# Kernel optimization log

Hardware: AMD Instinct MI355X
Metric: run time of the kernel (lower is better)

The kernel has to match this reference:

```python
import jax, jax.numpy as jnp
import numpy as np

D_MODEL = 256
NHEAD = 8
HEAD_DIM = D_MODEL // NHEAD
EPS = 1e-6
LN_EPS = 1e-5


def embed_rotary(x, cos, sin):
    # x, cos, sin: [N, L, C]; rotate even/odd pairs (Lepard-style RoFPE)
    x2 = jnp.stack([-x[..., 1::2], x[..., ::2]], axis=-1).reshape(x.shape)
    return x * cos + x2 * sin


def layer_norm(x, g, b):
    m = jnp.mean(x, axis=-1, keepdims=True)
    v = jnp.mean((x - m) ** 2, axis=-1, keepdims=True)
    return (x - m) / jnp.sqrt(v + LN_EPS) * g + b


def setup_inputs() -> dict:
    key = jax.random.key(0)
    ks = jax.random.split(key, 12)
    N, L, S, C = 8, 4096, 4096, D_MODEL
    s = 1.0 / np.sqrt(C)
    return {
        "x": jax.random.normal(ks[0], (N, L, C), jnp.float32),
        "source": jax.random.normal(ks[1], (N, S, C), jnp.float32),
        "x_pe": jax.random.normal(ks[2], (N, L, C, 2), jnp.float32),
        "source_pe": jax.random.normal(ks[3], (N, S, C, 2), jnp.float32),
        "Wq": jax.random.normal(ks[4], (C, C), jnp.float32) * s,
        "Wk": jax.random.normal(ks[5], (C, C), jnp.float32) * s,
        "Wv": jax.random.normal(ks[6], (C, C), jnp.float32) * s,
        "Wm": jax.random.normal(ks[7], (C, C), jnp.float32) * s,
        "W1": jax.random.normal(ks[8], (2 * C, 2 * C), jnp.float32) * s,
        "W2": jax.random.normal(ks[9], (2 * C, C), jnp.float32) * s,
        "ln1_g": jnp.ones((C,), jnp.float32),
        "ln1_b": jnp.zeros((C,), jnp.float32),
        "ln2_g": jnp.ones((C,), jnp.float32),
        "ln2_b": jnp.zeros((C,), jnp.float32),
    }


def reference(x, source, x_pe, source_pe, Wq, Wk, Wv, Wm, W1, W2, ln1_g, ln1_b, ln2_g, ln2_b):
    N, L, C = x.shape
    S = source.shape[1]
    H, D = NHEAD, HEAD_DIM

    query = x @ Wq           # [N, L, C]
    key = source @ Wk        # [N, S, C]
    value = source @ Wv      # [N, S, C]

    # ELU+1 feature maps (on pre-rotary projections)
    Q = jax.nn.elu(query) + 1.0
    K = jax.nn.elu(key) + 1.0

    q_cos, q_sin = x_pe[..., 0], x_pe[..., 1]
    k_cos, k_sin = source_pe[..., 0], source_pe[..., 1]
    Q_pos = embed_rotary(query, q_cos, q_sin)
    K_pos = embed_rotary(key, k_cos, k_sin)
    value = embed_rotary(value, k_cos, k_sin)

    Q = Q.reshape(N, L, H, D)
    K = K.reshape(N, S, H, D)
    Q_pos = Q_pos.reshape(N, L, H, D)
    K_pos = K_pos.reshape(N, S, H, D)
    value = value.reshape(N, S, H, D)

    values = value / S
    KV = jnp.einsum('nshd,nshv->nhdv', K_pos, values)          # [N, H, D, D]
    Z = 1.0 / (jnp.einsum('nlhd,nhd->nlh', Q, K.sum(axis=1)) + EPS)
    queried = jnp.einsum('nlhd,nhdv->nlhv', Q_pos, KV) * Z[..., None] * S  # [N, L, H, D]

    message = queried.reshape(N, L, C) @ Wm
    message = layer_norm(message, ln1_g, ln1_b)
    h = jnp.concatenate([x, message], axis=2) @ W1             # [N, L, 2C]
    h = jax.nn.relu(h)
    message = h @ W2                                            # [N, L, C]
    message = layer_norm(message, ln2_g, ln2_b)
    return x + message
```

## Files before the change

kernel.cpp:

```cpp
#include <hip/hip_runtime.h>

typedef __attribute__((ext_vector_type(8))) short bf16x8;
typedef __attribute__((ext_vector_type(4))) float f32x4;

__device__ __forceinline__ float bf2f(unsigned short b) {
    unsigned u = ((unsigned)b) << 16; float f;
    __builtin_memcpy(&f, &u, 4); return f;
}
__device__ __forceinline__ unsigned short f2bf(float f) {
    unsigned u; __builtin_memcpy(&u, &f, 4);
    unsigned r = u + 0x7FFFu + ((u >> 16) & 1u);
    return (unsigned short)(r >> 16);
}
__device__ __forceinline__ unsigned packbf(float a, float b) {
    return (unsigned)f2bf(a) | ((unsigned)f2bf(b) << 16);
}
__device__ __forceinline__ float elu1(float v) { return v > 0.f ? v + 1.f : __expf(v); }

__device__ __forceinline__ void async_copy16(const unsigned short* g, unsigned short* l) {
    __builtin_amdgcn_global_load_lds(
        (const __attribute__((address_space(1))) unsigned int*)g,
        (__attribute__((address_space(3))) unsigned int*)l, 16, 0, 0);
}

__device__ __host__ __forceinline__ int chan_of(int tc) {
    return (tc & ~63) | ((tc & 15) << 1) | ((tc >> 4) & 1) | (((tc >> 5) & 1) << 5);
}
__device__ __forceinline__ int chan_even(int gnb, int p, int low) {
    const int tc = gnb + 32 * p + low;
    return (tc & ~63) | ((tc & 15) << 1) | (((tc >> 5) & 1) << 5);
}

#define EPI_RELU 0
#define EPI_Q 1
#define EPI_KV 2
#define EPI_LN1 3
#define EPI_LN2RES 4

template <int MT, int NT, int EPI>
__global__ __launch_bounds__(256) void gemm_bt(
    const unsigned short* __restrict__ A, int lda,
    const unsigned short* __restrict__ B, int K,
    unsigned short* __restrict__ Cb, int ldc,
    const float* __restrict__ pe,
    const float* __restrict__ KsumC, float* __restrict__ KsumA,
    float* __restrict__ Zbuf, unsigned short* __restrict__ Qpos,
    unsigned short* __restrict__ KF, unsigned short* __restrict__ VF,
    const float* __restrict__ g, const float* __restrict__ bta,
    unsigned short* __restrict__ A2out,
    const float* __restrict__ xres, float* __restrict__ outF)
{
    constexpr int WM = MT / 2, WN = NT / 2, MI = WM / 16, NI = WN / 16;
    constexpr int LPS = 1 + NT / 64;
    constexpr int PF = (NT == 128) ? 4 : 2;
    constexpr int RD = PF + 1;
    static_assert(MT == 64, "A staging assumes MT*4 == 256 chunks");
    __shared__ unsigned short Asm[RD][MT * 32];
    __shared__ unsigned short Bsm[RD][NT * 32];
    const int t = threadIdx.x;
    const int lane = t & 63, w = t >> 6;
    const int wm = w & 1, wn = w >> 1;
    const int quad = lane >> 4, low = lane & 15;
    const int m0 = blockIdx.x * MT, n0 = blockIdx.y * NT;

    f32x4 acc[MI][NI];
#pragma unroll
    for (int i = 0; i < MI; i++)
#pragma unroll
        for (int j = 0; j < NI; j++) acc[i][j] = (f32x4){0.f, 0.f, 0.f, 0.f};

    auto stage = [&](int k0, int buf) {
        {
            const int row = t >> 2;
            const int part = (t & 3) ^ ((t >> 3) & 3);
            async_copy16(A + (size_t)(m0 + row) * lda + k0 + part * 8,
                         &Asm[buf][(w * 64) * 8]);
        }
#pragma unroll
        for (int i = 0; i < NT / 64; i++) {
            const int chunk = i * 256 + t;
            const int row = chunk >> 2;
            const int part = (chunk & 3) ^ ((chunk >> 3) & 3);
            async_copy16(B + (size_t)(n0 + row) * K + k0 + part * 8,
                         &Bsm[buf][(i * 256 + w * 64) * 8]);
        }
    };

    const int nk = K >> 5;
    const int swz = (low >> 1) & 3;
#pragma unroll
    for (int i = 0; i < PF; i++) stage(i << 5, i);
    int kb = 0, sb = PF;
    for (int ks = 0; ks < nk; ks++) {
        const int rem = nk - 1 - ks;
        __builtin_amdgcn_sched_barrier(0);
        if constexpr (PF == 4) {
            if (rem >= 3)      asm volatile("s_waitcnt vmcnt(9)" ::: "memory");
            else if (rem == 2) asm volatile("s_waitcnt vmcnt(6)" ::: "memory");
            else if (rem == 1) asm volatile("s_waitcnt vmcnt(3)" ::: "memory");
            else               asm volatile("s_waitcnt vmcnt(0)" ::: "memory");
        } else {
            if (rem >= 1)      asm volatile("s_waitcnt vmcnt(5)" ::: "memory");
            else               asm volatile("s_waitcnt vmcnt(0)" ::: "memory");
        }
        __builtin_amdgcn_s_barrier();
        __builtin_amdgcn_sched_barrier(0);
        if (ks + PF < nk) stage((ks + PF) << 5, sb);
        bf16x8 a[MI], b[NI];
#pragma unroll
        for (int mi = 0; mi < MI; mi++)
            a[mi] = *(const bf16x8*)&Asm[kb][(wm * WM + mi * 16 + low) * 32 + ((quad ^ swz)) * 8];
#pragma unroll
        for (int ni = 0; ni < NI; ni++)
            b[ni] = *(const bf16x8*)&Bsm[kb][(wn * WN + ni * 16 + low) * 32 + ((quad ^ swz)) * 8];
#pragma unroll
        for (int mi = 0; mi < MI; mi++)
#pragma unroll
            for (int ni = 0; ni < NI; ni++)
                acc[mi][ni] = __builtin_amdgcn_mfma_f32_16x16x32_bf16(a[mi], b[ni], acc[mi][ni], 0, 0, 0);
        kb = (kb + 1 == RD) ? 0 : kb + 1;
        sb = (sb + 1 == RD) ? 0 : sb + 1;
    }

    const int gmb = m0 + wm * WM, gnb = n0 + wn * WN;

    if constexpr (EPI == EPI_RELU) {
#pragma unroll
        for (int mi = 0; mi < MI; mi++)
#pragma unroll
            for (int p = 0; p < NI / 2; p++) {
                const int c_e = chan_even(gnb, p, low);
#pragma unroll
                for (int r = 0; r < 4; r++) {
                    const int row = gmb + mi * 16 + quad * 4 + r;
                    const float ve = acc[mi][2 * p][r], vo = acc[mi][2 * p + 1][r];
                    *(unsigned*)&Cb[(size_t)row * ldc + c_e] =
                        packbf(ve > 0.f ? ve : 0.f, vo > 0.f ? vo : 0.f);
                }
            }
    } else if constexpr (EPI == EPI_Q) {
        const int n = m0 >> 12;
#pragma unroll
        for (int p = 0; p < NI / 2; p++) {
            const int c_e = chan_even(gnb, p, low);
            const int head = c_e >> 5;
            const float2 ks = *(const float2*)&KsumC[n * 256 + c_e];
#pragma unroll
            for (int mi = 0; mi < MI; mi++) {
#pragma unroll
                for (int r = 0; r < 4; r++) {
                    const int row = gmb + mi * 16 + quad * 4 + r;
                    const float4 cs = *(const float4*)&pe[((size_t)row * 256 + c_e) * 2];
                    const float ve = acc[mi][2 * p][r], vo = acc[mi][2 * p + 1][r];
                    *(unsigned*)&Qpos[(size_t)row * 256 + c_e] =
                        packbf(ve * cs.x - vo * cs.y, vo * cs.z + ve * cs.w);
                    float z = elu1(ve) * ks.x + elu1(vo) * ks.y;
                    z += __shfl_xor(z, 1); z += __shfl_xor(z, 2);
                    z += __shfl_xor(z, 4); z += __shfl_xor(z, 8);
                    if (low == 0) Zbuf[(size_t)row * 8 + head] = 1.f / (z + 1e-6f);
                }
            }
        }
    } else if constexpr (EPI == EPI_KV) {
        const int n = m0 >> 12;
#pragma unroll
        for (int p = 0; p < NI / 2; p++) {
            const int tcg = gnb + 32 * p;
            const bool isK = ((tcg >> 5) & 1) == 0;
            const int c = ((tcg & ~63) >> 1) | (low << 1);
            const int nh = n * 8 + (c >> 5), d = c & 31;
            unsigned short* dst = isK ? KF : VF;
            float kel_e = 0.f, kel_o = 0.f;
#pragma unroll
            for (int mi = 0; mi < MI; mi++) {
                const int row0 = gmb + mi * 16 + quad * 4;
                const int s0 = row0 & 4095;
                unsigned short pk[8];
#pragma unroll
                for (int r = 0; r < 4; r++) {
                    const int row = row0 + r;
                    const float4 cs = *(const float4*)&pe[((size_t)row * 256 + c) * 2];
                    const float ve = acc[mi][2 * p][r], vo = acc[mi][2 * p + 1][r];
                    pk[r]     = f2bf(ve * cs.x - vo * cs.y);
                    pk[4 + r] = f2bf(vo * cs.z + ve * cs.w);
                    if (isK) { kel_e += elu1(ve); kel_o += elu1(vo); }
                }
                const size_t base = ((size_t)nh * 512 + (s0 >> 3)) * 32;
                *(uint2*)&dst[(base + d) * 8 + (s0 & 7)]     = *(const uint2*)&pk[0];
                *(uint2*)&dst[(base + d + 1) * 8 + (s0 & 7)] = *(const uint2*)&pk[4];
            }
            if (isK) {
                kel_e += __shfl_xor(kel_e, 16); kel_e += __shfl_xor(kel_e, 32);
                kel_o += __shfl_xor(kel_o, 16); kel_o += __shfl_xor(kel_o, 32);
                if (quad == 0) {
                    atomicAdd(&KsumA[n * 256 + c], kel_e);
                    atomicAdd(&KsumA[n * 256 + c + 1], kel_o);
                }
            }
        }
    } else {
        __shared__ float2 lnp[2][64];
#pragma unroll
        for (int mi = 0; mi < MI; mi++)
#pragma unroll
            for (int r = 0; r < 4; r++) {
                float s1 = 0.f, s2 = 0.f;
#pragma unroll
                for (int ni = 0; ni < NI; ni++) {
                    const float v = acc[mi][ni][r];
                    s1 += v; s2 += v * v;
                }
                s1 += __shfl_xor(s1, 1); s2 += __shfl_xor(s2, 1);
                s1 += __shfl_xor(s1, 2); s2 += __shfl_xor(s2, 2);
                s1 += __shfl_xor(s1, 4); s2 += __shfl_xor(s2, 4);
                s1 += __shfl_xor(s1, 8); s2 += __shfl_xor(s2, 8);
                if (low == 0) lnp[wn][wm * WM + mi * 16 + quad * 4 + r] = make_float2(s1, s2);
            }
        __syncthreads();
#pragma unroll
        for (int mi = 0; mi < MI; mi++)
#pragma unroll
            for (int r = 0; r < 4; r++) {
                const int rl = wm * WM + mi * 16 + quad * 4 + r;
                const int row = m0 + rl;
                const float2 pa = lnp[0][rl], pb = lnp[1][rl];
                const float mean = (pa.x + pb.x) * (1.f / 256.f);
                const float var = (pa.y + pb.y) * (1.f / 256.f) - mean * mean;
                const float rstd = rsqrtf(var + 1e-5f);
#pragma unroll
                for (int p = 0; p < NI / 2; p++) {
                    const int c_e = chan_even(gnb, p, low);
                    const float2 gg = *(const float2*)&g[c_e];
                    const float2 bb = *(const float2*)&bta[c_e];
                    const float ve = acc[mi][2 * p][r], vo = acc[mi][2 * p + 1][r];
                    const float oe = (ve - mean) * rstd * gg.x + bb.x;
                    const float oo = (vo - mean) * rstd * gg.y + bb.y;
                    if constexpr (EPI == EPI_LN1) {
                        *(unsigned*)&A2out[(size_t)row * 512 + 256 + c_e] = packbf(oe, oo);
                    } else {
                        const float2 xv = *(const float2*)&xres[(size_t)row * 256 + c_e];
                        float2 o; o.x = xv.x + oe; o.y = xv.y + oo;
                        *(float2*)&outF[(size_t)row * 256 + c_e] = o;
                    }
                }
            }
    }
}

__global__ void prep_weights(const float* __restrict__ Wq, const float* __restrict__ Wk,
                             const float* __restrict__ Wv, const float* __restrict__ Wm,
                             const float* __restrict__ W1, const float* __restrict__ W2,
                             unsigned short* __restrict__ WqT, unsigned short* __restrict__ WkvT,
                             unsigned short* __restrict__ WmT, unsigned short* __restrict__ W1T,
                             unsigned short* __restrict__ W2T, float* __restrict__ zero_base) {
    const int idx = blockIdx.x * 256 + threadIdx.x;
    if (idx < 65536) {
        const int tc = idx >> 8, k = idx & 255;
        WqT[idx] = f2bf(Wq[(size_t)k * 256 + chan_of(tc)]);
    } else if (idx < 196608) {
        const int i = idx - 65536, tc = i >> 8, k = i & 255;
        const int f = (tc >> 5) & 1;
        const int c = ((tc & ~63) >> 1) | ((tc & 15) << 1) | ((tc >> 4) & 1);
        WkvT[i] = f2bf(f ? Wv[(size_t)k * 256 + c] : Wk[(size_t)k * 256 + c]);
    } else if (idx < 262144) {
        const int i = idx - 196608, tc = i >> 8, k = i & 255;
        WmT[i] = f2bf(Wm[(size_t)k * 256 + chan_of(tc)]);
    } else if (idx < 524288) {
        const int i = idx - 262144, tc = i >> 9, k = i & 511;
        W1T[i] = f2bf(W1[(size_t)k * 512 + chan_of(tc)]);
    } else if (idx < 655360) {
        const int i = idx - 524288, tc = i >> 9, k = i & 511;
        W2T[i] = f2bf(W2[(size_t)k * 256 + chan_of(tc)]);
    } else {
        zero_base[idx - 655360] = 0.f;
    }
}

__global__ void conv_bf16(const float* __restrict__ src, unsigned short* __restrict__ dst, int dstride) {
    const int idx = blockIdx.x * 256 + threadIdx.x;
    const int row = idx >> 6;
    const int c0 = (idx & 63) * 4;
    const float4 v = *(const float4*)&src[(size_t)row * 256 + c0];
    unsigned short o[4] = {f2bf(v.x), f2bf(v.y), f2bf(v.z), f2bf(v.w)};
    *(uint2*)&dst[(size_t)row * dstride + c0] = *(const uint2*)o;
}

__global__ __launch_bounds__(256) void kv2_kernel(const unsigned short* __restrict__ KF,
                                                  const unsigned short* __restrict__ VF,
                                                  float* __restrict__ KVT) {
    const int nh = blockIdx.x, sc = blockIdx.y;
    const int t = threadIdx.x, lane = t & 63, w = t >> 6;
    const int quad = lane >> 4, low = lane & 15;
    const int sbase = sc * 1024 + w * 256;

    f32x4 acc[2][2];
#pragma unroll
    for (int i = 0; i < 2; i++)
#pragma unroll
        for (int j = 0; j < 2; j++) acc[i][j] = (f32x4){0.f, 0.f, 0.f, 0.f};

    for (int s0 = 0; s0 < 256; s0 += 32) {
        const int sk = sbase + s0 + quad * 8;
        const size_t cb = ((size_t)nh * 512 + (sk >> 3)) * 32;
        bf16x8 a[2], b[2];
#pragma unroll
        for (int mi = 0; mi < 2; mi++)
            a[mi] = *(const bf16x8*)&KF[(cb + mi * 16 + low) * 8];
#pragma unroll
        for (int ni = 0; ni < 2; ni++)
            b[ni] = *(const bf16x8*)&VF[(cb + ni * 16 + low) * 8];
#pragma unroll
        for (int mi = 0; mi < 2; mi++)
#pragma unroll
            for (int ni = 0; ni < 2; ni++)
                acc[mi][ni] = __builtin_amdgcn_mfma_f32_16x16x32_bf16(a[mi], b[ni], acc[mi][ni], 0, 0, 0);
    }

    __shared__ float red[4][1024];
#pragma unroll
    for (int mi = 0; mi < 2; mi++)
#pragma unroll
        for (int ni = 0; ni < 2; ni++)
#pragma unroll
            for (int r = 0; r < 4; r++)
                red[w][(mi * 16 + quad * 4 + r) * 32 + ni * 16 + low] = acc[mi][ni][r];
    __syncthreads();
#pragma unroll
    for (int k = 0; k < 4; k++) {
        const int i = t + k * 256;
        const float s = red[0][i] + red[1][i] + red[2][i] + red[3][i];
        atomicAdd(&KVT[(size_t)nh * 1024 + (size_t)(i & 31) * 32 + (i >> 5)], s);
    }
}

__global__ __launch_bounds__(256) void attn_out_kernel(const unsigned short* __restrict__ Qpos,
                                                       const float* __restrict__ KVT,
                                                       const float* __restrict__ Zbuf,
                                                       unsigned short* __restrict__ Qrd) {
    const int h = blockIdx.y, mt = blockIdx.x;
    const int t = threadIdx.x, lane = t & 63, w = t >> 6;
    const int quad = lane >> 4, low = lane & 15;
    const int rbase = mt * 256 + w * 64;
    const int n = rbase >> 12;

    bf16x8 b[2];
#pragma unroll
    for (int ni = 0; ni < 2; ni++) {
        const float* src = &KVT[((size_t)(n * 8 + h) * 32 + ni * 16 + low) * 32 + quad * 8];
        short tmp[8];
#pragma unroll
        for (int j = 0; j < 8; j++) tmp[j] = (short)f2bf(src[j]);
        __builtin_memcpy(&b[ni], tmp, 16);
    }

    f32x4 acc[4][2];
#pragma unroll
    for (int i = 0; i < 4; i++)
#pragma unroll
        for (int j = 0; j < 2; j++) acc[i][j] = (f32x4){0.f, 0.f, 0.f, 0.f};

#pragma unroll
    for (int mi = 0; mi < 4; mi++) {
        const bf16x8 a = *(const bf16x8*)&Qpos[((size_t)(rbase + mi * 16 + low)) * 256 + h * 32 + quad * 8];
#pragma unroll
        for (int ni = 0; ni < 2; ni++)
            acc[mi][ni] = __builtin_amdgcn_mfma_f32_16x16x32_bf16(a, b[ni], acc[mi][ni], 0, 0, 0);
    }

#pragma unroll
    for (int mi = 0; mi < 4; mi++)
#pragma unroll
        for (int ni = 0; ni < 2; ni++)
#pragma unroll
            for (int r = 0; r < 4; r++) {
                const int row = rbase + mi * 16 + quad * 4 + r;
                const int col = h * 32 + ni * 16 + low;
                Qrd[(size_t)row * 256 + col] = f2bf(acc[mi][ni][r] * Zbuf[(size_t)row * 8 + h]);
            }
}

extern "C" void kernel_launch(void* const* d_in, const int* in_sizes, int n_in,
                              void* d_out, int out_size, void* d_ws, size_t ws_size,
                              hipStream_t stream) {
    const float* x   = (const float*)d_in[0];
    const float* src = (const float*)d_in[1];
    const float* xpe = (const float*)d_in[2];
    const float* spe = (const float*)d_in[3];
    const float* Wq  = (const float*)d_in[4];
    const float* Wk  = (const float*)d_in[5];
    const float* Wv  = (const float*)d_in[6];
    const float* Wm  = (const float*)d_in[7];
    const float* W1  = (const float*)d_in[8];
    const float* W2  = (const float*)d_in[9];
    const float* g1  = (const float*)d_in[10];
    const float* b1  = (const float*)d_in[11];
    const float* g2  = (const float*)d_in[12];
    const float* b2  = (const float*)d_in[13];

    char* p = (char*)d_ws;
    unsigned short* WqT  = (unsigned short*)p; p += 256 * 256 * 2;
    unsigned short* WkvT = (unsigned short*)p; p += 512 * 256 * 2;
    unsigned short* WmT  = (unsigned short*)p; p += 256 * 256 * 2;
    unsigned short* W1T  = (unsigned short*)p; p += 512 * 512 * 2;
    unsigned short* W2T  = (unsigned short*)p; p += 256 * 512 * 2;
    float* KVT  = (float*)p; p += 64 * 1024 * 4;
    float* Ksum = (float*)p; p += 8 * 256 * 4;
    float* Zbuf = (float*)p; p += (size_t)32768 * 8 * 4;
    unsigned short* A2   = (unsigned short*)p; p += (size_t)32768 * 512 * 2;
    unsigned short* srcB = (unsigned short*)p; p += (size_t)32768 * 256 * 2;
    unsigned short* KF   = (unsigned short*)p; p += (size_t)32768 * 256 * 2;
    unsigned short* VF   = (unsigned short*)p; p += (size_t)32768 * 256 * 2;
    unsigned short* Qpos = (unsigned short*)p; p += (size_t)32768 * 256 * 2;
    unsigned short* Qrd  = (unsigned short*)p; p += (size_t)32768 * 256 * 2;
    unsigned short* hbuf = KF;

    prep_weights<<<2824, 256, 0, stream>>>(Wq, Wk, Wv, Wm, W1, W2,
                                           WqT, WkvT, WmT, W1T, W2T, KVT);
    conv_bf16<<<8192, 256, 0, stream>>>(x, A2, 512);
    conv_bf16<<<8192, 256, 0, stream>>>(src, srcB, 256);

    gemm_bt<64, 128, EPI_KV><<<dim3(512, 4), 256, 0, stream>>>(
        srcB, 256, WkvT, 256, nullptr, 0, spe, nullptr, Ksum,
        nullptr, nullptr, KF, VF, nullptr, nullptr, nullptr, nullptr, nullptr);
    kv2_kernel<<<dim3(64, 4), 256, 0, stream>>>(KF, VF, KVT);

    gemm_bt<64, 128, EPI_Q><<<dim3(512, 2), 256, 0, stream>>>(
        A2, 512, WqT, 256, nullptr, 0, xpe, Ksum, nullptr,
        Zbuf, Qpos, nullptr, nullptr, nullptr, nullptr, nullptr, nullptr, nullptr);

    attn_out_kernel<<<dim3(128, 8), 256, 0, stream>>>(Qpos, KVT, Zbuf, Qrd);

    gemm_bt<64, 256, EPI_LN1><<<512, 256, 0, stream>>>(
        Qrd, 256, WmT, 256, nullptr, 0, nullptr, nullptr, nullptr,
        nullptr, nullptr, nullptr, nullptr, g1, b1, A2, nullptr, nullptr);

    gemm_bt<64, 128, EPI_RELU><<<dim3(512, 4), 256, 0, stream>>>(
        A2, 512, W1T, 512, hbuf, 512, nullptr, nullptr, nullptr,
        nullptr, nullptr, nullptr, nullptr, nullptr, nullptr, nullptr, nullptr, nullptr);

    gemm_bt<64, 256, EPI_LN2RES><<<512, 256, 0, stream>>>(
        hbuf, 512, W2T, 512, nullptr, 0, nullptr, nullptr, nullptr,
        nullptr, nullptr, nullptr, nullptr, g2, b2, nullptr, x, (float*)d_out);
}
```

Before: 414.6 us.

## Fuse FFN W1+ReLU and W2+LayerNorm+residual into one kernel with LDS hidden tile

Replaces the two separate FFN GEMM launches with a single 512-thread kernel. Each block computes a 64x512 ReLU hidden tile into swizzled LDS, then multiplies it by W2 and applies LayerNorm and the residual add. This removes the 32 MB bf16 hidden-activation round trip through global memory and one launch. In exchange it uses large LDS (about 136 KB per block), which limits occupancy, and it uses shallow double buffering with full vmcnt(0) waits. It also changes the prefetch depth for NT=128 GEMMs from 4 to 2 and adjusts the wait counts to match.

```diff
diff --git a/kernel.cpp b/kernel.cpp
--- a/kernel.cpp
+++ b/kernel.cpp
@@ -31,28 +31,24 @@
     return (tc & ~63) | ((tc & 15) << 1) | (((tc >> 5) & 1) << 5);
 }
 
-#define EPI_RELU 0
 #define EPI_Q 1
 #define EPI_KV 2
 #define EPI_LN1 3
-#define EPI_LN2RES 4
 
 template <int MT, int NT, int EPI>
 __global__ __launch_bounds__(256) void gemm_bt(
     const unsigned short* __restrict__ A, int lda,
     const unsigned short* __restrict__ B, int K,
-    unsigned short* __restrict__ Cb, int ldc,
     const float* __restrict__ pe,
     const float* __restrict__ KsumC, float* __restrict__ KsumA,
     float* __restrict__ Zbuf, unsigned short* __restrict__ Qpos,
     unsigned short* __restrict__ KF, unsigned short* __restrict__ VF,
     const float* __restrict__ g, const float* __restrict__ bta,
-    unsigned short* __restrict__ A2out,
-    const float* __restrict__ xres, float* __restrict__ outF)
+    unsigned short* __restrict__ A2out)
 {
     constexpr int WM = MT / 2, WN = NT / 2, MI = WM / 16, NI = WN / 16;
     constexpr int LPS = 1 + NT / 64;
-    constexpr int PF = (NT == 128) ? 4 : 2;
+    constexpr int PF = 2;
     constexpr int RD = PF + 1;
     static_assert(MT == 64, "A staging assumes MT*4 == 256 chunks");
     __shared__ unsigned short Asm[RD][MT * 32];
@@ -94,10 +90,8 @@
     for (int ks = 0; ks < nk; ks++) {
         const int rem = nk - 1 - ks;
         __builtin_amdgcn_sched_barrier(0);
-        if constexpr (PF == 4) {
-            if (rem >= 3)      asm volatile("s_waitcnt vmcnt(9)" ::: "memory");
-            else if (rem == 2) asm volatile("s_waitcnt vmcnt(6)" ::: "memory");
-            else if (rem == 1) asm volatile("s_waitcnt vmcnt(3)" ::: "memory");
+        if constexpr (LPS == 3) {
+            if (rem >= 1)      asm volatile("s_waitcnt vmcnt(3)" ::: "memory");
             else               asm volatile("s_waitcnt vmcnt(0)" ::: "memory");
         } else {
             if (rem >= 1)      asm volatile("s_waitcnt vmcnt(5)" ::: "memory");
@@ -124,21 +118,7 @@
 
     const int gmb = m0 + wm * WM, gnb = n0 + wn * WN;
 
-    if constexpr (EPI == EPI_RELU) {
-#pragma unroll
-        for (int mi = 0; mi < MI; mi++)
-#pragma unroll
-            for (int p = 0; p < NI / 2; p++) {
-                const int c_e = chan_even(gnb, p, low);
-#pragma unroll
-                for (int r = 0; r < 4; r++) {
-                    const int row = gmb + mi * 16 + quad * 4 + r;
-                    const float ve = acc[mi][2 * p][r], vo = acc[mi][2 * p + 1][r];
-                    *(unsigned*)&Cb[(size_t)row * ldc + c_e] =
-                        packbf(ve > 0.f ? ve : 0.f, vo > 0.f ? vo : 0.f);
-                }
-            }
-    } else if constexpr (EPI == EPI_Q) {
+    if constexpr (EPI == EPI_Q) {
         const int n = m0 >> 12;
 #pragma unroll
         for (int p = 0; p < NI / 2; p++) {
@@ -235,16 +215,174 @@
                     const float ve = acc[mi][2 * p][r], vo = acc[mi][2 * p + 1][r];
                     const float oe = (ve - mean) * rstd * gg.x + bb.x;
                     const float oo = (vo - mean) * rstd * gg.y + bb.y;
-                    if constexpr (EPI == EPI_LN1) {
-                        *(unsigned*)&A2out[(size_t)row * 512 + 256 + c_e] = packbf(oe, oo);
-                    } else {
-                        const float2 xv = *(const float2*)&xres[(size_t)row * 256 + c_e];
-                        float2 o; o.x = xv.x + oe; o.y = xv.y + oo;
-                        *(float2*)&outF[(size_t)row * 256 + c_e] = o;
-                    }
+                    *(unsigned*)&A2out[(size_t)row * 512 + 256 + c_e] = packbf(oe, oo);
                 }
             }
     }
+}
+
+__global__ __launch_bounds__(512) void ffn_kernel(
+    const unsigned short* __restrict__ A2,
+    const unsigned short* __restrict__ W1T,
+    const unsigned short* __restrict__ W2T,
+    const float* __restrict__ g, const float* __restrict__ bta,
+    const float* __restrict__ xres, float* __restrict__ outF)
+{
+    __shared__ unsigned short Hs[64 * 512];
+    __shared__ unsigned short Bst[2][512 * 32];
+    __shared__ unsigned short Ast[2][64 * 32];
+    __shared__ float2 lnp[4][64];
+    const int t = threadIdx.x;
+    const int lane = t & 63, w = t >> 6;
+    const int wm = w & 1, wn = w >> 1;
+    const int quad = lane >> 4, low = lane & 15;
+    const int m0 = blockIdx.x * 64;
+    const int swz = (low >> 1) & 3;
+
+    f32x4 acc[2][8];
+#pragma unroll
+    for (int i = 0; i < 2; i++)
+#pragma unroll
+        for (int j = 0; j < 8; j++) acc[i][j] = (f32x4){0.f, 0.f, 0.f, 0.f};
+
+    auto stage1 = [&](int k0, int buf) {
+        if (w < 4) {
+            const int row = t >> 2;
+            const int part = (t & 3) ^ ((t >> 3) & 3);
+            async_copy16(A2 + (size_t)(m0 + row) * 512 + k0 + part * 8,
+                         &Ast[buf][(w * 64) * 8]);
+        }
+#pragma unroll
+        for (int i = 0; i < 4; i++) {
+            const int chunk = i * 512 + t;
+            const int row = chunk >> 2;
+            const int part = (chunk & 3) ^ ((chunk >> 3) & 3);
+            async_copy16(W1T + (size_t)row * 512 + k0 + part * 8,
+                         &Bst[buf][(i * 512 + w * 64) * 8]);
+        }
+    };
+
+    stage1(0, 0);
+    for (int ks = 0; ks < 16; ks++) {
+        const int kb = ks & 1;
+        __builtin_amdgcn_sched_barrier(0);
+        asm volatile("s_waitcnt vmcnt(0)" ::: "memory");
+        __builtin_amdgcn_s_barrier();
+        __builtin_amdgcn_sched_barrier(0);
+        if (ks + 1 < 16) stage1((ks + 1) << 5, kb ^ 1);
+        bf16x8 a[2], b[8];
+#pragma unroll
+        for (int mi = 0; mi < 2; mi++)
+            a[mi] = *(const bf16x8*)&Ast[kb][(wm * 32 + mi * 16 + low) * 32 + (quad ^ swz) * 8];
+#pragma unroll
+        for (int ni = 0; ni < 8; ni++)
+            b[ni] = *(const bf16x8*)&Bst[kb][(wn * 128 + ni * 16 + low) * 32 + (quad ^ swz) * 8];
+#pragma unroll
+        for (int mi = 0; mi < 2; mi++)
+#pragma unroll
+            for (int ni = 0; ni < 8; ni++)
+                acc[mi][ni] = __builtin_amdgcn_mfma_f32_16x16x32_bf16(a[mi], b[ni], acc[mi][ni], 0, 0, 0);
+    }
+
+    const int gnb1 = wn * 128;
+#pragma unroll
+    for (int mi = 0; mi < 2; mi++)
+#pragma unroll
+        for (int p = 0; p < 4; p++) {
+            const int c_e = chan_even(gnb1, p, low);
+#pragma unroll
+            for (int r = 0; r < 4; r++) {
+                const int row = wm * 32 + mi * 16 + quad * 4 + r;
+                const float ve = acc[mi][2 * p][r], vo = acc[mi][2 * p + 1][r];
+                const int col = c_e ^ ((row & 7) << 3);
+                *(unsigned*)&Hs[row * 512 + col] =
+                    packbf(ve > 0.f ? ve : 0.f, vo > 0.f ? vo : 0.f);
+            }
+        }
+    __syncthreads();
+
+    f32x4 acc2[2][4];
+#pragma unroll
+    for (int i = 0; i < 2; i++)
+#pragma unroll
+        for (int j = 0; j < 4; j++) acc2[i][j] = (f32x4){0.f, 0.f, 0.f, 0.f};
+
+    auto stage2 = [&](int k0, int buf) {
+#pragma unroll
+        for (int i = 0; i < 2; i++) {
+            const int chunk = i * 512 + t;
+            const int row = chunk >> 2;
+            const int part = (chunk & 3) ^ ((chunk >> 3) & 3);
+            async_copy16(W2T + (size_t)row * 512 + k0 + part * 8,
+                         &Bst[buf][(i * 512 + w * 64) * 8]);
+        }
+    };
+
+    stage2(0, 0);
+    for (int ks = 0; ks < 16; ks++) {
+        const int kb = ks & 1;
+        __builtin_amdgcn_sched_barrier(0);
+        asm volatile("s_waitcnt vmcnt(0)" ::: "memory");
+        __builtin_amdgcn_s_barrier();
+        __builtin_amdgcn_sched_barrier(0);
+        if (ks + 1 < 16) stage2((ks + 1) << 5, kb ^ 1);
+        bf16x8 a[2], b[4];
+#pragma unroll
+        for (int mi = 0; mi < 2; mi++) {
+            const int row = wm * 32 + mi * 16 + low;
+            a[mi] = *(const bf16x8*)&Hs[row * 512 + ((ks * 32 + quad * 8) ^ ((row & 7) << 3))];
+        }
+#pragma unroll
+        for (int ni = 0; ni < 4; ni++)
+            b[ni] = *(const bf16x8*)&Bst[kb][(wn * 64 + ni * 16 + low) * 32 + (quad ^ swz) * 8];
+#pragma unroll
+        for (int mi = 0; mi < 2; mi++)
+#pragma unroll
+            for (int ni = 0; ni < 4; ni++)
+                acc2[mi][ni] = __builtin_amdgcn_mfma_f32_16x16x32_bf16(a[mi], b[ni], acc2[mi][ni], 0, 0, 0);
+    }
+
+#pragma unroll
+    for (int mi = 0; mi < 2; mi++)
+#pragma unroll
+        for (int r = 0; r < 4; r++) {
+            float s1 = 0.f, s2 = 0.f;
+#pragma unroll
+            for (int ni = 0; ni < 4; ni++) {
+                const float v = acc2[mi][ni][r];
+                s1 += v; s2 += v * v;
+            }
+            s1 += __shfl_xor(s1, 1); s2 += __shfl_xor(s2, 1);
+            s1 += __shfl_xor(s1, 2); s2 += __shfl_xor(s2, 2);
+            s1 += __shfl_xor(s1, 4); s2 += __shfl_xor(s2, 4);
+            s1 += __shfl_xor(s1, 8); s2 += __shfl_xor(s2, 8);
+            if (low == 0) lnp[wn][wm * 32 + mi * 16 + quad * 4 + r] = make_float2(s1, s2);
+        }
+    __syncthreads();
+#pragma unroll
+    for (int mi = 0; mi < 2; mi++)
+#pragma unroll
+        for (int r = 0; r < 4; r++) {
+            const int rl = wm * 32 + mi * 16 + quad * 4 + r;
+            const int row = m0 + rl;
+            const float2 p0 = lnp[0][rl], p1 = lnp[1][rl];
+            const float2 p2 = lnp[2][rl], p3 = lnp[3][rl];
+            const float mean = (p0.x + p1.x + p2.x + p3.x) * (1.f / 256.f);
+            const float var = (p0.y + p1.y + p2.y + p3.y) * (1.f / 256.f) - mean * mean;
+            const float rstd = rsqrtf(var + 1e-5f);
+#pragma unroll
+            for (int p = 0; p < 2; p++) {
+                const int c_e = chan_even(wn * 64, p, low);
+                const float2 gg = *(const float2*)&g[c_e];
+                const float2 bb = *(const float2*)&bta[c_e];
+                const float ve = acc2[mi][2 * p][r], vo = acc2[mi][2 * p + 1][r];
+                const float oe = (ve - mean) * rstd * gg.x + bb.x;
+                const float oo = (vo - mean) * rstd * gg.y + bb.y;
+                const float2 xv = *(const float2*)&xres[(size_t)row * 256 + c_e];
+                float2 o; o.x = xv.x + oe; o.y = xv.y + oo;
+                *(float2*)&outF[(size_t)row * 256 + c_e] = o;
+            }
+        }
 }
 
 __global__ void prep_weights(const float* __restrict__ Wq, const float* __restrict__ Wk,
@@ -412,7 +550,6 @@
     unsigned short* VF   = (unsigned short*)p; p += (size_t)32768 * 256 * 2;
     unsigned short* Qpos = (unsigned short*)p; p += (size_t)32768 * 256 * 2;
     unsigned short* Qrd  = (unsigned short*)p; p += (size_t)32768 * 256 * 2;
-    unsigned short* hbuf = KF;
 
     prep_weights<<<2824, 256, 0, stream>>>(Wq, Wk, Wv, Wm, W1, W2,
                                            WqT, WkvT, WmT, W1T, W2T, KVT);
@@ -420,25 +557,19 @@
     conv_bf16<<<8192, 256, 0, stream>>>(src, srcB, 256);
 
     gemm_bt<64, 128, EPI_KV><<<dim3(512, 4), 256, 0, stream>>>(
-        srcB, 256, WkvT, 256, nullptr, 0, spe, nullptr, Ksum,
-        nullptr, nullptr, KF, VF, nullptr, nullptr, nullptr, nullptr, nullptr);
+        srcB, 256, WkvT, 256, spe, nullptr, Ksum,
+        nullptr, nullptr, KF, VF, nullptr, nullptr, nullptr);
     kv2_kernel<<<dim3(64, 4), 256, 0, stream>>>(KF, VF, KVT);
 
     gemm_bt<64, 128, EPI_Q><<<dim3(512, 2), 256, 0, stream>>>(
-        A2, 512, WqT, 256, nullptr, 0, xpe, Ksum, nullptr,
-        Zbuf, Qpos, nullptr, nullptr, nullptr, nullptr, nullptr, nullptr, nullptr);
+        A2, 512, WqT, 256, xpe, Ksum, nullptr,
+        Zbuf, Qpos, nullptr, nullptr, nullptr, nullptr, nullptr);
 
     attn_out_kernel<<<dim3(128, 8), 256, 0, stream>>>(Qpos, KVT, Zbuf, Qrd);
 
     gemm_bt<64, 256, EPI_LN1><<<512, 256, 0, stream>>>(
-        Qrd, 256, WmT, 256, nullptr, 0, nullptr, nullptr, nullptr,
-        nullptr, nullptr, nullptr, nullptr, g1, b1, A2, nullptr, nullptr);
-
-    gemm_bt<64, 128, EPI_RELU><<<dim3(512, 4), 256, 0, stream>>>(
-        A2, 512, W1T, 512, hbuf, 512, nullptr, nullptr, nullptr,
-        nullptr, nullptr, nullptr, nullptr, nullptr, nullptr, nullptr, nullptr, nullptr);
-
-    gemm_bt<64, 256, EPI_LN2RES><<<512, 256, 0, stream>>>(
-        hbuf, 512, W2T, 512, nullptr, 0, nullptr, nullptr, nullptr,
-        nullptr, nullptr, nullptr, nullptr, g2, b2, nullptr, x, (float*)d_out);
-}
+        Qrd, 256, WmT, 256, nullptr, nullptr, nullptr,
+        nullptr, nullptr, nullptr, nullptr, g1, b1, A2);
+
+    ffn_kernel<<<512, 512, 0, stream>>>(A2, W1T, W2T, g2, b2, x, (float*)d_out);
+}
```

After: 378.1 us. 1.1x faster.
